# Kernel optimization log

Hardware: AMD Instinct MI355X
Metric: run time of the kernel (lower is better)

## Reference

```python
import jax, jax.numpy as jnp
import numpy as np

HIDDEN = 1152
N_HEADS = 4
N_KV = 1
HEAD_DIM = 256
EPS = 1e-6
B, S = 4, 2048
ROPE_THETA = 1000000.0


def _rms_norm(x, w):
    # x: [..., D] float32; Gemma-style (1 + w) scale
    xf = x.astype(jnp.float32)
    inv = jax.lax.rsqrt(jnp.mean(xf * xf, axis=-1, keepdims=True) + EPS)
    return (xf * inv * (1.0 + w.astype(jnp.float32))).astype(x.dtype)


def _apply_rope(x, cos, sin):
    # x: [B, H, S, D]; cos/sin: [S, D/2]
    d2 = x.shape[-1] // 2
    x1, x2 = x[..., :d2], x[..., d2:]
    cos = cos[None, None, :, :]
    sin = sin[None, None, :, :]
    xr = x1 * cos - x2 * sin
    xi = x1 * sin + x2 * cos
    return jnp.concatenate([xr, xi], axis=-1).astype(x.dtype)


def setup_inputs() -> dict:
    key = jax.random.key(0)
    k_h, k_qkv, k_qn, k_kn, k_o = jax.random.split(key, 5)
    hidden_states = jax.random.normal(k_h, (B, S, HIDDEN), dtype=jnp.float32)
    # causal additive mask [1,1,S,S]
    neg = jnp.finfo(jnp.float32).min
    causal = jnp.tril(jnp.ones((S, S), dtype=bool))
    attention_mask = jnp.where(causal, 0.0, neg)[None, None, :, :].astype(jnp.float32)
    # RoPE tables (complex freqs_cis split into cos/sin)
    inv_freq = 1.0 / (ROPE_THETA ** (np.arange(0, HEAD_DIM, 2, dtype=np.float32) / HEAD_DIM))
    ang = np.arange(S, dtype=np.float32)[:, None] * inv_freq[None, :]
    freqs_cos = jnp.asarray(np.cos(ang))
    freqs_sin = jnp.asarray(np.sin(ang))
    qkv_out = (N_HEADS + 2 * N_KV) * HEAD_DIM
    scale = HIDDEN ** -0.5
    w_qkv = jax.random.normal(k_qkv, (HIDDEN, qkv_out), dtype=jnp.float32) * scale
    w_o = jax.random.normal(k_o, (N_HEADS * HEAD_DIM, HIDDEN), dtype=jnp.float32) * (N_HEADS * HEAD_DIM) ** -0.5
    q_norm_w = jax.random.normal(k_qn, (HEAD_DIM,), dtype=jnp.float32) * 0.02
    k_norm_w = jax.random.normal(k_kn, (HEAD_DIM,), dtype=jnp.float32) * 0.02
    return {
        "hidden_states": hidden_states,
        "attention_mask": attention_mask,
        "freqs_cos": freqs_cos,
        "freqs_sin": freqs_sin,
        "w_qkv": w_qkv,
        "q_norm_w": q_norm_w,
        "k_norm_w": k_norm_w,
        "w_o": w_o,
    }


def reference(hidden_states, attention_mask, freqs_cos, freqs_sin, w_qkv, q_norm_w, k_norm_w, w_o):
    b, s, _ = hidden_states.shape
    groups = N_HEADS // N_KV
    scaling = HEAD_DIM ** -0.5

    qkv = jnp.einsum("bsh,ho->bso", hidden_states, w_qkv)
    q_end = N_HEADS * HEAD_DIM
    k_end = q_end + N_KV * HEAD_DIM
    q = qkv[:, :, :q_end].reshape(b, s, N_HEADS, HEAD_DIM).transpose(0, 2, 1, 3)
    k = qkv[:, :, q_end:k_end].reshape(b, s, N_KV, HEAD_DIM).transpose(0, 2, 1, 3)
    v = qkv[:, :, k_end:].reshape(b, s, N_KV, HEAD_DIM).transpose(0, 2, 1, 3)

    q = _rms_norm(q, q_norm_w)
    k = _rms_norm(k, k_norm_w)

    q = _apply_rope(q, freqs_cos, freqs_sin)
    k = _apply_rope(k, freqs_cos, freqs_sin)

    if groups > 1:
        k = jnp.repeat(k, groups, axis=1)  # [B, H, S, D]
        v = jnp.repeat(v, groups, axis=1)

    scores = jnp.einsum("bhqd,bhkd->bhqk", q * scaling, k)
    scores = scores + attention_mask.astype(jnp.float32)
    probs = jax.nn.softmax(scores.astype(jnp.float32), axis=-1).astype(q.dtype)

    attn = jnp.einsum("bhqk,bhkd->bhqd", probs, v)
    attn = attn.transpose(0, 2, 1, 3).reshape(b, s, N_HEADS * HEAD_DIM)
    return jnp.einsum("bsf,fh->bsh", attn, w_o)
```

## Files before the change

kernel.cpp:

```cpp
#include <hip/hip_runtime.h>

typedef _Float16 f16;
typedef _Float16 f16x8 __attribute__((ext_vector_type(8)));
typedef _Float16 f16x4 __attribute__((ext_vector_type(4)));
typedef float f32x4 __attribute__((ext_vector_type(4)));

#define NH 4
#define HD 256
#define BB 4
#define SS 2048
#define HID 1152
#define QKV_N 1536
#define ODIM (NH * HD)

#define OPART_OFF 33554432L
#define ML_OFF 81395712L

__global__ __launch_bounds__(256) void transpose_cvt(
    const float* __restrict__ src, long src_ld, long src_bs,
    f16* __restrict__ dst, long dst_ld, long dst_bs) {
  __shared__ float tile[32][33];
  src += (long)blockIdx.z * src_bs;
  dst += (long)blockIdx.z * dst_bs;
  int r0 = blockIdx.y * 32, c0 = blockIdx.x * 32;
  int tc = threadIdx.x & 31, tr = threadIdx.x >> 5;
#pragma unroll
  for (int i = 0; i < 4; ++i)
    tile[tr + i * 8][tc] = src[(long)(r0 + tr + i * 8) * src_ld + c0 + tc];
  __syncthreads();
#pragma unroll
  for (int i = 0; i < 4; ++i)
    dst[(long)(c0 + tr + i * 8) * dst_ld + r0 + tc] = (f16)tile[tc][tr + i * 8];
}

__global__ __launch_bounds__(256, 2) void gemm_a32_b16(
    const float* __restrict__ A, const f16* __restrict__ Bt,
    float* __restrict__ C, int K, int N) {
  __shared__ f16 As[128][40];
  __shared__ f16 Bs[128][40];
  int tid = threadIdx.x;
  int wave = tid >> 6, lane = tid & 63;
  int l16 = lane & 15, lhi = lane >> 4;
  int wm = (wave >> 1) * 64, wn = (wave & 1) * 64;
  long bm = (long)blockIdx.x * 128, bn = (long)blockIdx.y * 128;
  f32x4 acc[4][4] = {};
  int a_kq = (tid & 7) * 4, a_r = tid >> 3;
  int b_ko = (tid & 3) * 8, b_r = tid >> 2;

  for (int k0 = 0; k0 < K; k0 += 32) {
#pragma unroll
    for (int i = 0; i < 4; ++i) {
      int r = a_r + 32 * i;
      float4 v = *(const float4*)&A[(bm + r) * K + k0 + a_kq];
      f16x4 h = {(f16)v.x, (f16)v.y, (f16)v.z, (f16)v.w};
      *(f16x4*)&As[r][a_kq] = h;
    }
#pragma unroll
    for (int i = 0; i < 2; ++i) {
      int r = b_r + 64 * i;
      *(uint4*)&Bs[r][b_ko] = *(const uint4*)&Bt[(bn + r) * K + k0 + b_ko];
    }
    __syncthreads();
    f16x8 af[4], bf[4];
#pragma unroll
    for (int i = 0; i < 4; ++i)
      af[i] = *(const f16x8*)&As[wm + i * 16 + l16][lhi * 8];
#pragma unroll
    for (int j = 0; j < 4; ++j)
      bf[j] = *(const f16x8*)&Bs[wn + j * 16 + l16][lhi * 8];
#pragma unroll
    for (int i = 0; i < 4; ++i)
#pragma unroll
      for (int j = 0; j < 4; ++j)
        acc[i][j] = __builtin_amdgcn_mfma_f32_16x16x32_f16(af[i], bf[j], acc[i][j], 0, 0, 0);
    __syncthreads();
  }
#pragma unroll
  for (int i = 0; i < 4; ++i) {
    long row = bm + wm + i * 16 + lhi * 4;
#pragma unroll
    for (int r = 0; r < 4; ++r) {
      float* crow = C + (row + r) * N + bn + wn + l16;
#pragma unroll
      for (int j = 0; j < 4; ++j) crow[j * 16] = acc[i][j][r];
    }
  }
}

__device__ __forceinline__ void norm_rope_store(
    const float* __restrict__ x, const float* __restrict__ w,
    const float* __restrict__ fc, const float* __restrict__ fs,
    f16* __restrict__ dst, float scale, int lane) {
  float x0 = x[lane], x1 = x[lane + 64], x2 = x[lane + 128], x3 = x[lane + 192];
  float ss = x0 * x0 + x1 * x1 + x2 * x2 + x3 * x3;
#pragma unroll
  for (int m = 1; m < 64; m <<= 1) ss += __shfl_xor(ss, m, 64);
  float inv = rsqrtf(ss * (1.0f / 256.0f) + 1e-6f);
  x0 *= inv * (1.0f + w[lane]);
  x1 *= inv * (1.0f + w[lane + 64]);
  x2 *= inv * (1.0f + w[lane + 128]);
  x3 *= inv * (1.0f + w[lane + 192]);
  float c0 = fc[lane], s0 = fs[lane], c1 = fc[lane + 64], s1 = fs[lane + 64];
  dst[lane]       = (f16)((x0 * c0 - x2 * s0) * scale);
  dst[lane + 64]  = (f16)((x1 * c1 - x3 * s1) * scale);
  dst[lane + 128] = (f16)((x0 * s0 + x2 * c0) * scale);
  dst[lane + 192] = (f16)((x1 * s1 + x3 * c1) * scale);
}

__global__ __launch_bounds__(256) void qkv_post(
    const float* __restrict__ qkv, const float* __restrict__ qnw,
    const float* __restrict__ knw, const float* __restrict__ fcos,
    const float* __restrict__ fsin, f16* __restrict__ Q, f16* __restrict__ Kb) {
  long row = blockIdx.x;
  int b = (int)(row >> 11), s = (int)(row & 2047);
  int wave = threadIdx.x >> 6, lane = threadIdx.x & 63;
  const float* base = qkv + row * QKV_N;
  const float* fc = fcos + (long)s * 128;
  const float* fs = fsin + (long)s * 128;
  norm_rope_store(base + wave * HD, qnw, fc, fs,
                  Q + ((long)(b * NH + wave) * SS + s) * HD, 0.0625f, lane);
  if (wave == 0)
    norm_rope_store(base + NH * HD, knw, fc, fs, Kb + row * HD, 1.0f, lane);
}

__global__ __launch_bounds__(256, 3) void attn_fwd(
    const f16* __restrict__ Q, const f16* __restrict__ Kb,
    const f16* __restrict__ Vt, float* __restrict__ O,
    f16* __restrict__ Opart, float2* __restrict__ ml) {
  __shared__ f16 Klds[32][264];
  __shared__ f16 Vlds[256][40];
  __shared__ f16 Plds[4][16][40];
  int it = blockIdx.x, h = blockIdx.y, b = blockIdx.z;
  int qb, t0, t1, pidx = 0;
  bool split;
  if (it < 16) {
    qb = it; t0 = 0; t1 = 2 * qb + 2; split = false;
  } else {
    int j = it - 16;
    qb = 16 + (j >> 1);
    int s = j & 1, half = qb + 1;
    t0 = s * half; t1 = t0 + half; split = true;
    pidx = (((b * NH + h) << 4) + (qb - 16)) * 2 + s;
  }
  int tid = threadIdx.x, wave = tid >> 6, lane = tid & 63;
  int l16 = lane & 15, lhi = lane >> 4;
  int q0 = qb * 64 + wave * 16;

  const f16* Kg = Kb + (long)b * SS * HD;
  const f16* Vg = Vt + (long)b * HD * SS;

  f16x8 qf[8];
  const f16* Qbase = Q + ((long)(b * NH + h) * SS + q0 + l16) * HD + lhi * 8;
#pragma unroll
  for (int kb = 0; kb < 8; ++kb) qf[kb] = *(const f16x8*)(Qbase + kb * 32);

  f32x4 o[16] = {};
  float m_i = -1e30f, l_i = 0.f;

  int kr = tid >> 5, kc = (tid & 31) * 8;
  int rv = tid >> 2, vc = (tid & 3) * 8;

  for (int t = t0; t < t1; ++t) {
    int kv0 = t * 32;
    __syncthreads();
#pragma unroll
    for (int i = 0; i < 4; ++i)
      *(uint4*)&Klds[kr + i * 8][kc] =
          *(const uint4*)(Kg + (long)(kv0 + kr + i * 8) * HD + kc);
#pragma unroll
    for (int i = 0; i < 4; ++i)
      *(uint4*)&Vlds[rv + i * 64][vc] =
          *(const uint4*)(Vg + (long)(rv + i * 64) * SS + kv0 + vc);
    __syncthreads();

    f32x4 sc[2] = {};
#pragma unroll
    for (int kb = 0; kb < 8; ++kb) {
#pragma unroll
      for (int cf = 0; cf < 2; ++cf) {
        f16x8 kf = *(const f16x8*)&Klds[cf * 16 + l16][kb * 32 + lhi * 8];
        sc[cf] = __builtin_amdgcn_mfma_f32_16x16x32_f16(kf, qf[kb], sc[cf], 0, 0, 0);
      }
    }

    float p[8];
    float mx = -1e30f;
    int qrow = q0 + l16;
    if (t >= 2 * qb) {
#pragma unroll
      for (int cf = 0; cf < 2; ++cf)
#pragma unroll
        for (int r = 0; r < 4; ++r) {
          int kv = kv0 + cf * 16 + lhi * 4 + r;
          float s = (kv <= qrow) ? sc[cf][r] : -1e30f;
          p[cf * 4 + r] = s;
          mx = fmaxf(mx, s);
        }
    } else {
#pragma unroll
      for (int i = 0; i < 8; ++i) {
        float s = sc[i >> 2][i & 3];
        p[i] = s;
        mx = fmaxf(mx, s);
      }
    }
    mx = fmaxf(mx, __shfl_xor(mx, 16));
    mx = fmaxf(mx, __shfl_xor(mx, 32));
    float mn = fmaxf(m_i, mx);
    float scl = __expf(m_i - mn);
    float rs = 0.f;
#pragma unroll
    for (int i = 0; i < 8; ++i) {
      p[i] = __expf(p[i] - mn);
      rs += p[i];
    }
    rs += __shfl_xor(rs, 16);
    rs += __shfl_xor(rs, 32);
    l_i = l_i * scl + rs;
    m_i = mn;

#pragma unroll
    for (int cf = 0; cf < 2; ++cf) {
      f16x4 hp = {(f16)p[cf * 4], (f16)p[cf * 4 + 1], (f16)p[cf * 4 + 2],
                  (f16)p[cf * 4 + 3]};
      *(f16x4*)&Plds[wave][l16][cf * 16 + lhi * 4] = hp;
    }

    float s0 = __shfl(scl, lhi * 4 + 0);
    float s1 = __shfl(scl, lhi * 4 + 1);
    float s2 = __shfl(scl, lhi * 4 + 2);
    float s3 = __shfl(scl, lhi * 4 + 3);
#pragma unroll
    for (int nf = 0; nf < 16; ++nf) {
      o[nf][0] *= s0;
      o[nf][1] *= s1;
      o[nf][2] *= s2;
      o[nf][3] *= s3;
    }

    f16x8 pa = *(const f16x8*)&Plds[wave][l16][lhi * 8];
#pragma unroll
    for (int nf = 0; nf < 16; ++nf) {
      f16x8 vf = *(const f16x8*)&Vlds[nf * 16 + l16][lhi * 8];
      o[nf] = __builtin_amdgcn_mfma_f32_16x16x32_f16(pa, vf, o[nf], 0, 0, 0);
    }
  }

  float inv = 1.0f / l_i;
  float i0 = __shfl(inv, lhi * 4 + 0);
  float i1 = __shfl(inv, lhi * 4 + 1);
  float i2 = __shfl(inv, lhi * 4 + 2);
  float i3 = __shfl(inv, lhi * 4 + 3);
  float ir[4] = {i0, i1, i2, i3};
  if (!split) {
#pragma unroll
    for (int r = 0; r < 4; ++r) {
      long srow = q0 + lhi * 4 + r;
      float* Orow = O + ((long)b * SS + srow) * ODIM + h * HD + l16;
#pragma unroll
      for (int nf = 0; nf < 16; ++nf) Orow[nf * 16] = o[nf][r] * ir[r];
    }
  } else {
#pragma unroll
    for (int r = 0; r < 4; ++r) {
      int rloc = wave * 16 + lhi * 4 + r;
      f16* Prow = Opart + ((long)pidx * 64 + rloc) * HD + l16;
#pragma unroll
      for (int nf = 0; nf < 16; ++nf) Prow[nf * 16] = (f16)(o[nf][r] * ir[r]);
    }
    if (lane < 16) {
      float2 v; v.x = m_i; v.y = l_i;
      ml[(long)pidx * 64 + wave * 16 + lane] = v;
    }
  }
}

__global__ __launch_bounds__(256) void attn_combine(
    const f16* __restrict__ Opart, const float2* __restrict__ ml,
    float* __restrict__ O) {
  int qx = blockIdx.x, h = blockIdx.y, b = blockIdx.z;
  int qb = 16 + qx;
  int p0 = (((b * NH + h) << 4) + qx) * 2;
  int tid = threadIdx.x;
  int r = tid >> 2, d0 = (tid & 3) * 64;
  float2 a = ml[(long)p0 * 64 + r];
  float2 c = ml[(long)(p0 + 1) * 64 + r];
  float M = fmaxf(a.x, c.x);
  float w0 = a.y * __expf(a.x - M), w1 = c.y * __expf(c.x - M);
  float invL = 1.0f / (w0 + w1);
  w0 *= invL; w1 *= invL;
  const f16* o0 = Opart + ((long)p0 * 64 + r) * HD + d0;
  const f16* o1 = Opart + ((long)(p0 + 1) * 64 + r) * HD + d0;
  float* Orow = O + ((long)b * SS + qb * 64 + r) * ODIM + h * HD + d0;
#pragma unroll
  for (int i = 0; i < 8; ++i) {
    f16x8 x = *(const f16x8*)(o0 + i * 8);
    f16x8 y = *(const f16x8*)(o1 + i * 8);
#pragma unroll
    for (int j = 0; j < 8; ++j)
      Orow[i * 8 + j] = w0 * (float)x[j] + w1 * (float)y[j];
  }
}

extern "C" void kernel_launch(void* const* d_in, const int* in_sizes, int n_in,
                              void* d_out, int out_size, void* d_ws, size_t ws_size,
                              hipStream_t stream) {
  const float* hidden = (const float*)d_in[0];
  const float* fcos = (const float*)d_in[2];
  const float* fsin = (const float*)d_in[3];
  const float* wqkv = (const float*)d_in[4];
  const float* qnw = (const float*)d_in[5];
  const float* knw = (const float*)d_in[6];
  const float* wo = (const float*)d_in[7];
  float* out = (float*)d_out;

  char* ws = (char*)d_ws;
  float* qkv = (float*)(ws + 0);
  float* Obuf = (float*)(ws + 0);
  f16* Opart = (f16*)(ws + OPART_OFF);
  f16* Qb = (f16*)(ws + 50331648);
  f16* Kb = (f16*)(ws + 67108864);
  f16* Vt = (f16*)(ws + 71303168);
  f16* wqkvt = (f16*)(ws + 75497472);
  f16* wot = (f16*)(ws + 79036416);
  float2* ml = (float2*)(ws + ML_OFF);

  transpose_cvt<<<dim3(QKV_N / 32, HID / 32, 1), 256, 0, stream>>>(
      wqkv, QKV_N, 0, wqkvt, HID, 0);
  transpose_cvt<<<dim3(HID / 32, ODIM / 32, 1), 256, 0, stream>>>(
      wo, HID, 0, wot, ODIM, 0);

  gemm_a32_b16<<<dim3(BB * SS / 128, QKV_N / 128), 256, 0, stream>>>(
      hidden, wqkvt, qkv, HID, QKV_N);

  qkv_post<<<dim3(BB * SS), 256, 0, stream>>>(qkv, qnw, knw, fcos, fsin, Qb, Kb);

  transpose_cvt<<<dim3(HD / 32, SS / 32, BB), 256, 0, stream>>>(
      qkv + 1280, QKV_N, (long)SS * QKV_N, Vt, SS, (long)HD * SS);

  attn_fwd<<<dim3(48, NH, BB), 256, 0, stream>>>(Qb, Kb, Vt, Obuf, Opart, ml);

  attn_combine<<<dim3(16, NH, BB), 256, 0, stream>>>(Opart, ml, Obuf);

  gemm_a32_b16<<<dim3(BB * SS / 128, HID / 128), 256, 0, stream>>>(
      Obuf, wot, out, ODIM, HID);
}
```

Measured before the change: 238.4 us.

## Keep intermediates in fp16 and rewrite GEMM with direct global-to-LDS loads

The hidden states are converted to fp16 in a separate pass. Both GEMMs now take fp16 A operands, and the QKV projection and attention output are stored as fp16 instead of fp32, which roughly halves the intermediate memory traffic. The GEMM is rewritten to use global_load_lds 16-byte transfers with a K-tile of 64, unpadded LDS, occupancy hint 3, and vectorized epilogue stores. Risks include LDS bank conflicts from the unpadded tiles, fp16 rounding of the QKV intermediate, and the cost of the extra conversion kernel.

```diff
diff --git a/kernel.cpp b/kernel.cpp
--- a/kernel.cpp
+++ b/kernel.cpp
@@ -13,11 +13,38 @@
 #define QKV_N 1536
 #define ODIM (NH * HD)
 
+#define QKV16_OFF 0L
+#define HID16_OFF 25165824L
+#define OBUF_OFF 0L
 #define OPART_OFF 33554432L
+#define QB_OFF 50331648L
+#define KB_OFF 67108864L
+#define VT_OFF 71303168L
+#define WQKVT_OFF 75497472L
+#define WOT_OFF 79036416L
 #define ML_OFF 81395712L
 
+#define GLL16(gp, lp)                                                      \
+  __builtin_amdgcn_global_load_lds(                                       \
+      (const __attribute__((address_space(1))) char*)(gp),                \
+      (__attribute__((address_space(3))) char*)(lp), 16, 0, 0)
+
+__global__ __launch_bounds__(256) void cvt_f32_to_f16(
+    const float* __restrict__ s, f16* __restrict__ d, long n) {
+  long i = ((long)blockIdx.x * 256 + threadIdx.x) * 8;
+  long stride = (long)gridDim.x * 256 * 8;
+  for (; i < n; i += stride) {
+    float4 a = *(const float4*)(s + i);
+    float4 b = *(const float4*)(s + i + 4);
+    f16x8 h = {(f16)a.x, (f16)a.y, (f16)a.z, (f16)a.w,
+               (f16)b.x, (f16)b.y, (f16)b.z, (f16)b.w};
+    *(f16x8*)(d + i) = h;
+  }
+}
+
+template <typename ST>
 __global__ __launch_bounds__(256) void transpose_cvt(
-    const float* __restrict__ src, long src_ld, long src_bs,
+    const ST* __restrict__ src, long src_ld, long src_bs,
     f16* __restrict__ dst, long dst_ld, long dst_bs) {
   __shared__ float tile[32][33];
   src += (long)blockIdx.z * src_bs;
@@ -26,72 +53,80 @@
   int tc = threadIdx.x & 31, tr = threadIdx.x >> 5;
 #pragma unroll
   for (int i = 0; i < 4; ++i)
-    tile[tr + i * 8][tc] = src[(long)(r0 + tr + i * 8) * src_ld + c0 + tc];
+    tile[tr + i * 8][tc] = (float)src[(long)(r0 + tr + i * 8) * src_ld + c0 + tc];
   __syncthreads();
 #pragma unroll
   for (int i = 0; i < 4; ++i)
     dst[(long)(c0 + tr + i * 8) * dst_ld + r0 + tc] = (f16)tile[tc][tr + i * 8];
 }
 
-__global__ __launch_bounds__(256, 2) void gemm_a32_b16(
-    const float* __restrict__ A, const f16* __restrict__ Bt,
-    float* __restrict__ C, int K, int N) {
-  __shared__ f16 As[128][40];
-  __shared__ f16 Bs[128][40];
-  int tid = threadIdx.x;
-  int wave = tid >> 6, lane = tid & 63;
+template <typename CT>
+__global__ __launch_bounds__(256, 3) void gemm_f16(
+    const f16* __restrict__ A, const f16* __restrict__ Bt,
+    CT* __restrict__ C, int K, int N) {
+  __shared__ f16 As[128][64];
+  __shared__ f16 Bs[128][64];
+  int tid = threadIdx.x, wave = tid >> 6, lane = tid & 63;
   int l16 = lane & 15, lhi = lane >> 4;
   int wm = (wave >> 1) * 64, wn = (wave & 1) * 64;
   long bm = (long)blockIdx.x * 128, bn = (long)blockIdx.y * 128;
   f32x4 acc[4][4] = {};
-  int a_kq = (tid & 7) * 4, a_r = tid >> 3;
-  int b_ko = (tid & 3) * 8, b_r = tid >> 2;
-
-  for (int k0 = 0; k0 < K; k0 += 32) {
-#pragma unroll
-    for (int i = 0; i < 4; ++i) {
-      int r = a_r + 32 * i;
-      float4 v = *(const float4*)&A[(bm + r) * K + k0 + a_kq];
-      f16x4 h = {(f16)v.x, (f16)v.y, (f16)v.z, (f16)v.w};
-      *(f16x4*)&As[r][a_kq] = h;
-    }
-#pragma unroll
-    for (int i = 0; i < 2; ++i) {
-      int r = b_r + 64 * i;
-      *(uint4*)&Bs[r][b_ko] = *(const uint4*)&Bt[(bn + r) * K + k0 + b_ko];
-    }
+
+  int srow = wave * 32 + (lane >> 3);
+  int scol = (lane & 7) * 8;
+  const f16* Ag = A + (bm + srow) * (long)K + scol;
+  const f16* Bg = Bt + (bn + srow) * (long)K + scol;
+
+  for (int k0 = 0; k0 < K; k0 += 64) {
+#pragma unroll
+    for (int i = 0; i < 4; ++i)
+      GLL16(Ag + k0 + (long)i * 8 * K, &As[wave * 32 + i * 8][0]);
+#pragma unroll
+    for (int i = 0; i < 4; ++i)
+      GLL16(Bg + k0 + (long)i * 8 * K, &Bs[wave * 32 + i * 8][0]);
     __syncthreads();
-    f16x8 af[4], bf[4];
-#pragma unroll
-    for (int i = 0; i < 4; ++i)
-      af[i] = *(const f16x8*)&As[wm + i * 16 + l16][lhi * 8];
-#pragma unroll
-    for (int j = 0; j < 4; ++j)
-      bf[j] = *(const f16x8*)&Bs[wn + j * 16 + l16][lhi * 8];
-#pragma unroll
-    for (int i = 0; i < 4; ++i)
+#pragma unroll
+    for (int kb = 0; kb < 2; ++kb) {
+      f16x8 af[4], bf[4];
+#pragma unroll
+      for (int i = 0; i < 4; ++i)
+        af[i] = *(const f16x8*)&As[wm + i * 16 + l16][kb * 32 + lhi * 8];
 #pragma unroll
       for (int j = 0; j < 4; ++j)
-        acc[i][j] = __builtin_amdgcn_mfma_f32_16x16x32_f16(af[i], bf[j], acc[i][j], 0, 0, 0);
+        bf[j] = *(const f16x8*)&Bs[wn + j * 16 + l16][kb * 32 + lhi * 8];
+#pragma unroll
+      for (int i = 0; i < 4; ++i)
+#pragma unroll
+        for (int j = 0; j < 4; ++j)
+          acc[i][j] =
+              __builtin_amdgcn_mfma_f32_16x16x32_f16(bf[j], af[i], acc[i][j], 0, 0, 0);
+    }
     __syncthreads();
   }
+
 #pragma unroll
   for (int i = 0; i < 4; ++i) {
-    long row = bm + wm + i * 16 + lhi * 4;
-#pragma unroll
-    for (int r = 0; r < 4; ++r) {
-      float* crow = C + (row + r) * N + bn + wn + l16;
-#pragma unroll
-      for (int j = 0; j < 4; ++j) crow[j * 16] = acc[i][j][r];
+    long m = bm + wm + i * 16 + l16;
+#pragma unroll
+    for (int j = 0; j < 4; ++j) {
+      long n = bn + wn + j * 16 + lhi * 4;
+      if constexpr (sizeof(CT) == 2) {
+        f16x4 h = {(f16)acc[i][j][0], (f16)acc[i][j][1], (f16)acc[i][j][2],
+                   (f16)acc[i][j][3]};
+        *(f16x4*)&C[m * N + n] = h;
+      } else {
+        *(f32x4*)&C[m * N + n] = acc[i][j];
+      }
     }
   }
 }
 
 __device__ __forceinline__ void norm_rope_store(
-    const float* __restrict__ x, const float* __restrict__ w,
+    const f16* __restrict__ x, const float* __restrict__ w,
     const float* __restrict__ fc, const float* __restrict__ fs,
     f16* __restrict__ dst, float scale, int lane) {
-  float x0 = x[lane], x1 = x[lane + 64], x2 = x[lane + 128], x3 = x[lane + 192];
+  float x0 = (float)x[lane], x1 = (float)x[lane + 64];
+  float x2 = (float)x[lane + 128], x3 = (float)x[lane + 192];
   float ss = x0 * x0 + x1 * x1 + x2 * x2 + x3 * x3;
 #pragma unroll
   for (int m = 1; m < 64; m <<= 1) ss += __shfl_xor(ss, m, 64);
@@ -108,13 +143,13 @@
 }
 
 __global__ __launch_bounds__(256) void qkv_post(
-    const float* __restrict__ qkv, const float* __restrict__ qnw,
+    const f16* __restrict__ qkv, const float* __restrict__ qnw,
     const float* __restrict__ knw, const float* __restrict__ fcos,
     const float* __restrict__ fsin, f16* __restrict__ Q, f16* __restrict__ Kb) {
   long row = blockIdx.x;
   int b = (int)(row >> 11), s = (int)(row & 2047);
   int wave = threadIdx.x >> 6, lane = threadIdx.x & 63;
-  const float* base = qkv + row * QKV_N;
+  const f16* base = qkv + row * QKV_N;
   const float* fc = fcos + (long)s * 128;
   const float* fs = fsin + (long)s * 128;
   norm_rope_store(base + wave * HD, qnw, fc, fs,
@@ -125,7 +160,7 @@
 
 __global__ __launch_bounds__(256, 3) void attn_fwd(
     const f16* __restrict__ Q, const f16* __restrict__ Kb,
-    const f16* __restrict__ Vt, float* __restrict__ O,
+    const f16* __restrict__ Vt, f16* __restrict__ O,
     f16* __restrict__ Opart, float2* __restrict__ ml) {
   __shared__ f16 Klds[32][264];
   __shared__ f16 Vlds[256][40];
@@ -256,9 +291,9 @@
 #pragma unroll
     for (int r = 0; r < 4; ++r) {
       long srow = q0 + lhi * 4 + r;
-      float* Orow = O + ((long)b * SS + srow) * ODIM + h * HD + l16;
-#pragma unroll
-      for (int nf = 0; nf < 16; ++nf) Orow[nf * 16] = o[nf][r] * ir[r];
+      f16* Orow = O + ((long)b * SS + srow) * ODIM + h * HD + l16;
+#pragma unroll
+      for (int nf = 0; nf < 16; ++nf) Orow[nf * 16] = (f16)(o[nf][r] * ir[r]);
     }
   } else {
 #pragma unroll
@@ -277,7 +312,7 @@
 
 __global__ __launch_bounds__(256) void attn_combine(
     const f16* __restrict__ Opart, const float2* __restrict__ ml,
-    float* __restrict__ O) {
+    f16* __restrict__ O) {
   int qx = blockIdx.x, h = blockIdx.y, b = blockIdx.z;
   int qb = 16 + qx;
   int p0 = (((b * NH + h) << 4) + qx) * 2;
@@ -291,14 +326,16 @@
   w0 *= invL; w1 *= invL;
   const f16* o0 = Opart + ((long)p0 * 64 + r) * HD + d0;
   const f16* o1 = Opart + ((long)(p0 + 1) * 64 + r) * HD + d0;
-  float* Orow = O + ((long)b * SS + qb * 64 + r) * ODIM + h * HD + d0;
+  f16* Orow = O + ((long)b * SS + qb * 64 + r) * ODIM + h * HD + d0;
 #pragma unroll
   for (int i = 0; i < 8; ++i) {
     f16x8 x = *(const f16x8*)(o0 + i * 8);
     f16x8 y = *(const f16x8*)(o1 + i * 8);
+    f16x8 z;
 #pragma unroll
     for (int j = 0; j < 8; ++j)
-      Orow[i * 8 + j] = w0 * (float)x[j] + w1 * (float)y[j];
+      z[j] = (f16)(w0 * (float)x[j] + w1 * (float)y[j]);
+    *(f16x8*)(Orow + i * 8) = z;
   }
 }
 
@@ -315,33 +352,35 @@
   float* out = (float*)d_out;
 
   char* ws = (char*)d_ws;
-  float* qkv = (float*)(ws + 0);
-  float* Obuf = (float*)(ws + 0);
+  f16* qkv16 = (f16*)(ws + QKV16_OFF);
+  f16* hid16 = (f16*)(ws + HID16_OFF);
+  f16* Obuf = (f16*)(ws + OBUF_OFF);
   f16* Opart = (f16*)(ws + OPART_OFF);
-  f16* Qb = (f16*)(ws + 50331648);
-  f16* Kb = (f16*)(ws + 67108864);
-  f16* Vt = (f16*)(ws + 71303168);
-  f16* wqkvt = (f16*)(ws + 75497472);
-  f16* wot = (f16*)(ws + 79036416);
+  f16* Qb = (f16*)(ws + QB_OFF);
+  f16* Kb = (f16*)(ws + KB_OFF);
+  f16* Vt = (f16*)(ws + VT_OFF);
+  f16* wqkvt = (f16*)(ws + WQKVT_OFF);
+  f16* wot = (f16*)(ws + WOT_OFF);
   float2* ml = (float2*)(ws + ML_OFF);
 
-  transpose_cvt<<<dim3(QKV_N / 32, HID / 32, 1), 256, 0, stream>>>(
+  cvt_f32_to_f16<<<2048, 256, 0, stream>>>(hidden, hid16, (long)BB * SS * HID);
+
+  transpose_cvt<float><<<dim3(QKV_N / 32, HID / 32, 1), 256, 0, stream>>>(
       wqkv, QKV_N, 0, wqkvt, HID, 0);
-  transpose_cvt<<<dim3(HID / 32, ODIM / 32, 1), 256, 0, stream>>>(
+  transpose_cvt<float><<<dim3(HID / 32, ODIM / 32, 1), 256, 0, stream>>>(
       wo, HID, 0, wot, ODIM, 0);
 
-  gemm_a32_b16<<<dim3(BB * SS / 128, QKV_N / 128), 256, 0, stream>>>(
-      hidden, wqkvt, qkv, HID, QKV_N);
-
-  qkv_post<<<dim3(BB * SS), 256, 0, stream>>>(qkv, qnw, knw, fcos, fsin, Qb, Kb);
-
-  transpose_cvt<<<dim3(HD / 32, SS / 32, BB), 256, 0, stream>>>(
-      qkv + 1280, QKV_N, (long)SS * QKV_N, Vt, SS, (long)HD * SS);
+  gemm_f16<f16><<<dim3(BB * SS / 128, QKV_N / 128), 256, 0, stream>>>(
+      hid16, wqkvt, qkv16, HID, QKV_N);
+
+  qkv_post<<<dim3(BB * SS), 256, 0, stream>>>(qkv16, qnw, knw, fcos, fsin, Qb, Kb);
+
+  transpose_cvt<f16><<<dim3(HD / 32, SS / 32, BB), 256, 0, stream>>>(
+      qkv16 + 1280, QKV_N, (long)SS * QKV_N, Vt, SS, (long)HD * SS);
 
   attn_fwd<<<dim3(48, NH, BB), 256, 0, stream>>>(Qb, Kb, Vt, Obuf, Opart, ml);
-
   attn_combine<<<dim3(16, NH, BB), 256, 0, stream>>>(Opart, ml, Obuf);
 
-  gemm_a32_b16<<<dim3(BB * SS / 128, HID / 128), 256, 0, stream>>>(
+  gemm_f16<float><<<dim3(BB * SS / 128, HID / 128), 256, 0, stream>>>(
       Obuf, wot, out, ODIM, HID);
 }
```

After: 237.0 us. About the same (-0.6%).
